# Optimization experiments

Hardware: AMD Instinct MI355X
Metric: run time of the kernel (lower is better)

## Reference

```python
import jax, jax.numpy as jnp
import numpy as np

NSLICES = 4
HID = 512
IN_DIM = 342   # input_shape - 1 (last column is phase)
OUT_DIM = 311
BATCH = 1024


def _cubic(y0, y1, y2, y3, mu):
    mu2 = mu * mu
    mu3 = mu2 * mu
    return ((-0.5 * y0 + 1.5 * y1 - 1.5 * y2 + 0.5 * y3) * mu3
            + (y0 - 2.5 * y1 + 2.0 * y2 - 0.5 * y3) * mu2
            + (-0.5 * y0 + 0.5 * y2) * mu
            + y1)


def setup_inputs() -> dict:
    key = jax.random.key(0)
    kx, k0, k1, k2 = jax.random.split(key, 4)
    x = jax.random.uniform(kx, (BATCH, IN_DIM + 1), dtype=jnp.float32)
    W0 = jax.random.normal(k0, (NSLICES, HID, IN_DIM), dtype=jnp.float32) * 0.1
    W1 = jax.random.normal(k1, (NSLICES, HID, HID), dtype=jnp.float32) * 0.1
    W2 = jax.random.normal(k2, (NSLICES, OUT_DIM, HID), dtype=jnp.float32) * 0.1
    b0 = jnp.zeros((NSLICES, HID), dtype=jnp.float32)
    b1 = jnp.zeros((NSLICES, HID), dtype=jnp.float32)
    b2 = jnp.zeros((NSLICES, OUT_DIM), dtype=jnp.float32)
    return {"x": x, "W0": W0, "W1": W1, "W2": W2, "b0": b0, "b1": b1, "b2": b2}


def reference(x, W0, W1, W2, b0, b1, b2):
    data, phase = x[:, :-1], x[:, -1]          # [B, 342], [B]
    pscale = NSLICES * phase                    # phase in [0,1) -> pscale in [0,4)
    mu = pscale % 1.0                           # [B]
    i1 = pscale.astype(jnp.int32) % NSLICES
    i0 = (i1 - 1) % NSLICES
    i2 = (i1 + 1) % NSLICES
    i3 = (i1 + 2) % NSLICES

    muW = mu[:, None, None]
    mub = mu[:, None]

    # Per-sample interpolated weights/biases (gather 4 slices + cubic blend)
    W0i = _cubic(W0[i0], W0[i1], W0[i2], W0[i3], muW)   # [B, 512, 342]
    W1i = _cubic(W1[i0], W1[i1], W1[i2], W1[i3], muW)   # [B, 512, 512]
    W2i = _cubic(W2[i0], W2[i1], W2[i2], W2[i3], muW)   # [B, 311, 512]
    b0i = _cubic(b0[i0], b0[i1], b0[i2], b0[i3], mub)   # [B, 512]
    b1i = _cubic(b1[i0], b1[i1], b1[i2], b1[i3], mub)   # [B, 512]
    b2i = _cubic(b2[i0], b2[i1], b2[i2], b2[i3], mub)   # [B, 311]

    # 3-layer MLP with per-sample weights (batched GEMV); dropout in eval mode (identity)
    H1 = jax.nn.elu(jnp.einsum('boi,bi->bo', W0i, data) + b0i)
    H2 = jax.nn.elu(jnp.einsum('boi,bi->bo', W1i, H1) + b1i)
    H3 = jnp.einsum('boi,bi->bo', W2i, H2) + b2i
    return H3
```

## Files before the change

kernel.cpp:

```cpp
#include <hip/hip_runtime.h>
#include <hip/hip_fp16.h>
#include <math.h>

typedef _Float16 f16x8 __attribute__((ext_vector_type(8)));
typedef float f32x4 __attribute__((ext_vector_type(4)));

#define NS 4
#define HID 512
#define IN_DIM 342
#define OUT_DIM 311
#define BATCH 1024
#define INP 352
#define K0V (NS*INP)
#define K12V (NS*HID)
#define XROW (IN_DIM+1)

#define OFF_ACOEF 0
#define OFF_X0H   4096
#define OFF_W0H   (OFF_X0H + 720896)
#define OFF_W1H   (OFF_W0H + 360448)
#define OFF_W2H   (OFF_W1H + 524288)
#define OFF_H1X   (OFF_W2H + 327680)
#define OFF_H2X   OFF_X0H

typedef __attribute__((address_space(3))) void lds_t;
typedef __attribute__((address_space(1))) const void gvm_t;
__device__ __forceinline__ void gload16(const void* g, void* l) {
    __builtin_amdgcn_global_load_lds((gvm_t*)g, (lds_t*)l, 16, 0, 0);
}

__global__ __launch_bounds__(256) void prep_all(
    const float* __restrict__ x,
    const float* __restrict__ W0, const float* __restrict__ W1,
    const float* __restrict__ W2,
    float* __restrict__ acoef,
    __half* __restrict__ X0h, __half* __restrict__ W0h,
    __half* __restrict__ W1h, __half* __restrict__ W2h)
{
    const int bid = blockIdx.x;
    const int t = threadIdx.x;
    if (bid < 512) {
        int o = bid;
        for (int k = t; k < K0V; k += 256) {
            int s = k / INP;
            int i = k - s*INP;
            float v = 0.f;
            if (i < IN_DIM) v = W0[((size_t)s*HID + o)*IN_DIM + i];
            W0h[(size_t)o*K0V + k] = __float2half(v);
        }
    } else if (bid < 1024) {
        int o = bid - 512;
        int k = t * 8;
        int s = k >> 9, i = k & 511;
        const float* src = W1 + ((size_t)s*HID + o)*HID + i;
        float4 v0 = *(const float4*)(src);
        float4 v1 = *(const float4*)(src + 4);
        f16x8 h;
        h[0]=(_Float16)v0.x; h[1]=(_Float16)v0.y; h[2]=(_Float16)v0.z; h[3]=(_Float16)v0.w;
        h[4]=(_Float16)v1.x; h[5]=(_Float16)v1.y; h[6]=(_Float16)v1.z; h[7]=(_Float16)v1.w;
        *(f16x8*)(W1h + (size_t)o*K12V + k) = h;
    } else if (bid < 1344) {
        int o = bid - 1024;
        int k = t * 8;
        int s = k >> 9, i = k & 511;
        f16x8 h = {};
        if (o < OUT_DIM) {
            const float* src = W2 + ((size_t)s*OUT_DIM + o)*HID + i;
            float4 v0 = *(const float4*)(src);
            float4 v1 = *(const float4*)(src + 4);
            h[0]=(_Float16)v0.x; h[1]=(_Float16)v0.y; h[2]=(_Float16)v0.z; h[3]=(_Float16)v0.w;
            h[4]=(_Float16)v1.x; h[5]=(_Float16)v1.y; h[6]=(_Float16)v1.z; h[7]=(_Float16)v1.w;
        }
        *(f16x8*)(W2h + (size_t)o*K12V + k) = h;
    } else {
        int b = bid - 1344;
        float phase = x[(size_t)b*XROW + IN_DIM];
        float ps = (float)NS * phase;
        float mu = ps - floorf(ps);
        int i1 = ((int)ps) & (NS-1);
        float mu2 = mu*mu, mu3 = mu2*mu;
        float c1 =  1.5f*mu3 - 2.5f*mu2 + 1.0f;
        float c2 = -1.5f*mu3 + 2.0f*mu2 + 0.5f*mu;
        float c3 =  0.5f*mu3 - 0.5f*mu2;
        float c0 = -0.5f*mu3 +      mu2 - 0.5f*mu;
        if (t < 4) {
            int rel = (t - i1) & 3;
            acoef[b*4 + t] = (rel==0)?c1:(rel==1)?c2:(rel==2)?c3:c0;
        }
        for (int k = t; k < K0V; k += 256) {
            int s = k / INP;
            int i = k - s*INP;
            int rel = (s - i1) & 3;
            float sel = (rel==0)?c1:(rel==1)?c2:(rel==2)?c3:c0;
            float v = (i < IN_DIM) ? x[(size_t)b*XROW + i] * sel : 0.f;
            X0h[(size_t)b*K0V + k] = __float2half(v);
        }
    }
}

template<int LAYER>
__global__ __launch_bounds__(256) void gemm_mfma(
    const __half* __restrict__ A,
    const __half* __restrict__ Bw,
    const float* __restrict__ acoef,
    const float* __restrict__ bias,
    __half* __restrict__ outH,
    float* __restrict__ outF)
{
    constexpr int K  = (LAYER==0) ? K0V : K12V;
    constexpr int NB = (LAYER==2) ? OUT_DIM : HID;
    constexpr int NITER = K / 128;

    __shared__ __align__(16) char lbuf[4][24576];

    const int t    = threadIdx.x;
    const int lane = t & 63;
    const int wid  = t >> 6;
    const int wm   = wid >> 1;
    const int wn   = wid & 1;
    const int m0   = blockIdx.y * 32;
    const int n0   = blockIdx.x * 64;

    const int cS = lane & 15;
    const int r4 = lane >> 4;
    const int rA0 = 4*(wid    ) + r4;
    const int rA1 = 4*(wid + 4) + r4;
    const __half* aSrc0 = A + (size_t)(m0 + rA0)*K + (((cS&8)|((cS&7)^(rA0&7))) * 8);
    const __half* aSrc1 = A + (size_t)(m0 + rA1)*K + (((cS&8)|((cS&7)^(rA1&7))) * 8);
    const int rB0 = 4*(wid     ) + r4;
    const int rB1 = 4*(wid +  4) + r4;
    const int rB2 = 4*(wid +  8) + r4;
    const int rB3 = 4*(wid + 12) + r4;
    const __half* bSrc0 = Bw + (size_t)(n0 + rB0)*K + (((cS&8)|((cS&7)^(rB0&7))) * 8);
    const __half* bSrc1 = Bw + (size_t)(n0 + rB1)*K + (((cS&8)|((cS&7)^(rB1&7))) * 8);
    const __half* bSrc2 = Bw + (size_t)(n0 + rB2)*K + (((cS&8)|((cS&7)^(rB2&7))) * 8);
    const __half* bSrc3 = Bw + (size_t)(n0 + rB3)*K + (((cS&8)|((cS&7)^(rB3&7))) * 8);

    f32x4 acc[2] = {};

    auto stage = [&](int it) {
        char* base = lbuf[it & 3];
        const int ko = it * 128;
        gload16(aSrc0 + ko, base + (wid    )*1024);
        gload16(aSrc1 + ko, base + (wid + 4)*1024);
        gload16(bSrc0 + ko, base + 8192 + (wid     )*1024);
        gload16(bSrc1 + ko, base + 8192 + (wid +  4)*1024);
        gload16(bSrc2 + ko, base + 8192 + (wid +  8)*1024);
        gload16(bSrc3 + ko, base + 8192 + (wid + 12)*1024);
    };

    stage(0);
    stage(1);
    stage(2);

    for (int it = 0; it < NITER; ++it) {
        if (it + 2 < NITER)      asm volatile("s_waitcnt vmcnt(12)" ::: "memory");
        else if (it + 1 < NITER) asm volatile("s_waitcnt vmcnt(6)"  ::: "memory");
        else                     asm volatile("s_waitcnt vmcnt(0)"  ::: "memory");
        __builtin_amdgcn_s_barrier();
        __builtin_amdgcn_sched_barrier(0);
        if (it + 3 < NITER) stage(it + 3);
        const char* sA = lbuf[it & 3];
        const char* sB = sA + 8192;
        #pragma unroll
        for (int kk = 0; kk < 4; ++kk) {
            const int kb = kk*64 + (lane>>4)*16;
            const int rr = wm*16 + (lane&15);
            f16x8 af = *(const f16x8*)(sA + rr*256 + (kb ^ ((rr&7)<<4)));
            #pragma unroll
            for (int ni = 0; ni < 2; ++ni) {
                const int oo = wn*32 + ni*16 + (lane&15);
                f16x8 bf = *(const f16x8*)(sB + oo*256 + (kb ^ ((oo&7)<<4)));
                acc[ni] = __builtin_amdgcn_mfma_f32_16x16x32_f16(af, bf, acc[ni], 0, 0, 0);
            }
        }
    }

    #pragma unroll
    for (int r = 0; r < 4; ++r) {
        const int row = m0 + wm*16 + (lane>>4)*4 + r;
        const float c0 = acoef[row*4+0], c1 = acoef[row*4+1],
                    c2 = acoef[row*4+2], c3 = acoef[row*4+3];
        #pragma unroll
        for (int ni = 0; ni < 2; ++ni) {
            const int col = n0 + wn*32 + ni*16 + (lane&15);
            float v = acc[ni][r];
            if (LAYER == 2) {
                if (col < OUT_DIM) {
                    float bi = c0*bias[col] + c1*bias[NB+col]
                             + c2*bias[2*NB+col] + c3*bias[3*NB+col];
                    outF[(size_t)row*OUT_DIM + col] = v + bi;
                }
            } else {
                float bi = c0*bias[col] + c1*bias[NB+col]
                         + c2*bias[2*NB+col] + c3*bias[3*NB+col];
                v += bi;
                v = (v > 0.f) ? v : expm1f(v);
                size_t o = (size_t)row*K12V + col;
                outH[o        ] = __float2half(c0*v);
                outH[o +   HID] = __float2half(c1*v);
                outH[o + 2*HID] = __float2half(c2*v);
                outH[o + 3*HID] = __float2half(c3*v);
            }
        }
    }
}

extern "C" void kernel_launch(void* const* d_in, const int* in_sizes, int n_in,
                              void* d_out, int out_size, void* d_ws, size_t ws_size,
                              hipStream_t stream) {
    const float* x  = (const float*)d_in[0];
    const float* W0 = (const float*)d_in[1];
    const float* W1 = (const float*)d_in[2];
    const float* W2 = (const float*)d_in[3];
    const float* b0 = (const float*)d_in[4];
    const float* b1 = (const float*)d_in[5];
    const float* b2 = (const float*)d_in[6];
    float* out = (float*)d_out;
    float* ws  = (float*)d_ws;

    float*  acoef = ws + OFF_ACOEF;
    __half* X0h   = (__half*)(ws + OFF_X0H);
    __half* W0h   = (__half*)(ws + OFF_W0H);
    __half* W1h   = (__half*)(ws + OFF_W1H);
    __half* W2h   = (__half*)(ws + OFF_W2H);
    __half* H1x   = (__half*)(ws + OFF_H1X);
    __half* H2x   = (__half*)(ws + OFF_H2X);

    prep_all<<<dim3(2368), dim3(256), 0, stream>>>(x, W0, W1, W2, acoef,
                                                   X0h, W0h, W1h, W2h);

    gemm_mfma<0><<<dim3(HID/64, BATCH/32), dim3(256), 0, stream>>>(
        X0h, W0h, acoef, b0, H1x, nullptr);
    gemm_mfma<1><<<dim3(HID/64, BATCH/32), dim3(256), 0, stream>>>(
        H1x, W1h, acoef, b1, H2x, nullptr);
    gemm_mfma<2><<<dim3(320/64, BATCH/32), dim3(256), 0, stream>>>(
        H2x, W2h, acoef, b2, nullptr, out);
}
```

Before: 38.39 us.

## Overlap W1/W2 fp16 conversion with layer-0 GEMM and vectorize X/W0 prep

The prep kernel now only converts X (scaled by the cubic coefficients) and W0, using 8-wide vectorized loads and stores instead of strided scalar loops. The W1 and W2 fp32-to-fp16 conversion moves into extra blocks appended to the layer-0 GEMM grid, so it runs alongside the GEMM tiles. This shortens the serial prep stage and hides the weight-conversion memory traffic behind layer-0 compute. In exchange, the layer-0 grid becomes heterogeneous, and the conversion blocks still allocate the GEMM's shared-memory footprint.

```diff
diff --git a/kernel.cpp b/kernel.cpp
--- a/kernel.cpp
+++ b/kernel.cpp
@@ -29,71 +29,68 @@
     __builtin_amdgcn_global_load_lds((gvm_t*)g, (lds_t*)l, 16, 0, 0);
 }
 
-__global__ __launch_bounds__(256) void prep_all(
+__global__ __launch_bounds__(256) void prep_xw0(
     const float* __restrict__ x,
-    const float* __restrict__ W0, const float* __restrict__ W1,
-    const float* __restrict__ W2,
+    const float* __restrict__ W0,
     float* __restrict__ acoef,
-    __half* __restrict__ X0h, __half* __restrict__ W0h,
-    __half* __restrict__ W1h, __half* __restrict__ W2h)
+    __half* __restrict__ X0h, __half* __restrict__ W0h)
 {
     const int bid = blockIdx.x;
     const int t = threadIdx.x;
     if (bid < 512) {
         int o = bid;
-        for (int k = t; k < K0V; k += 256) {
-            int s = k / INP;
-            int i = k - s*INP;
-            float v = 0.f;
-            if (i < IN_DIM) v = W0[((size_t)s*HID + o)*IN_DIM + i];
-            W0h[(size_t)o*K0V + k] = __float2half(v);
-        }
-    } else if (bid < 1024) {
-        int o = bid - 512;
-        int k = t * 8;
-        int s = k >> 9, i = k & 511;
-        const float* src = W1 + ((size_t)s*HID + o)*HID + i;
-        float4 v0 = *(const float4*)(src);
-        float4 v1 = *(const float4*)(src + 4);
-        f16x8 h;
-        h[0]=(_Float16)v0.x; h[1]=(_Float16)v0.y; h[2]=(_Float16)v0.z; h[3]=(_Float16)v0.w;
-        h[4]=(_Float16)v1.x; h[5]=(_Float16)v1.y; h[6]=(_Float16)v1.z; h[7]=(_Float16)v1.w;
-        *(f16x8*)(W1h + (size_t)o*K12V + k) = h;
-    } else if (bid < 1344) {
-        int o = bid - 1024;
-        int k = t * 8;
-        int s = k >> 9, i = k & 511;
-        f16x8 h = {};
-        if (o < OUT_DIM) {
-            const float* src = W2 + ((size_t)s*OUT_DIM + o)*HID + i;
-            float4 v0 = *(const float4*)(src);
-            float4 v1 = *(const float4*)(src + 4);
-            h[0]=(_Float16)v0.x; h[1]=(_Float16)v0.y; h[2]=(_Float16)v0.z; h[3]=(_Float16)v0.w;
-            h[4]=(_Float16)v1.x; h[5]=(_Float16)v1.y; h[6]=(_Float16)v1.z; h[7]=(_Float16)v1.w;
-        }
-        *(f16x8*)(W2h + (size_t)o*K12V + k) = h;
+        if (t < 176) {
+            int s = t / 44;
+            int cm = t - s*44;
+            int i = cm * 8;
+            const float* src = W0 + ((size_t)s*HID + o)*IN_DIM + i;
+            f16x8 h;
+            if (i + 8 <= IN_DIM) {
+                float4 v0 = *(const float4*)(src);
+                float4 v1 = *(const float4*)(src + 4);
+                h[0]=(_Float16)v0.x; h[1]=(_Float16)v0.y; h[2]=(_Float16)v0.z; h[3]=(_Float16)v0.w;
+                h[4]=(_Float16)v1.x; h[5]=(_Float16)v1.y; h[6]=(_Float16)v1.z; h[7]=(_Float16)v1.w;
+            } else {
+                #pragma unroll
+                for (int j=0;j<8;++j) h[j] = (_Float16)((i+j < IN_DIM) ? src[j] : 0.f);
+            }
+            *(f16x8*)(W0h + (size_t)o*K0V + t*8) = h;
+        }
     } else {
-        int b = bid - 1344;
+        int b = bid - 512;
         float phase = x[(size_t)b*XROW + IN_DIM];
         float ps = (float)NS * phase;
         float mu = ps - floorf(ps);
         int i1 = ((int)ps) & (NS-1);
         float mu2 = mu*mu, mu3 = mu2*mu;
-        float c1 =  1.5f*mu3 - 2.5f*mu2 + 1.0f;
-        float c2 = -1.5f*mu3 + 2.0f*mu2 + 0.5f*mu;
-        float c3 =  0.5f*mu3 - 0.5f*mu2;
-        float c0 = -0.5f*mu3 +      mu2 - 0.5f*mu;
+        float r0 =  1.5f*mu3 - 2.5f*mu2 + 1.0f;
+        float r1 = -1.5f*mu3 + 2.0f*mu2 + 0.5f*mu;
+        float r2 =  0.5f*mu3 - 0.5f*mu2;
+        float r3 = -0.5f*mu3 +      mu2 - 0.5f*mu;
         if (t < 4) {
             int rel = (t - i1) & 3;
-            acoef[b*4 + t] = (rel==0)?c1:(rel==1)?c2:(rel==2)?c3:c0;
-        }
-        for (int k = t; k < K0V; k += 256) {
-            int s = k / INP;
-            int i = k - s*INP;
+            acoef[b*4 + t] = (rel==0)?r0:(rel==1)?r1:(rel==2)?r2:r3;
+        }
+        if (t < 176) {
+            int s = t / 44;
+            int cm = t - s*44;
+            int i = cm * 8;
             int rel = (s - i1) & 3;
-            float sel = (rel==0)?c1:(rel==1)?c2:(rel==2)?c3:c0;
-            float v = (i < IN_DIM) ? x[(size_t)b*XROW + i] * sel : 0.f;
-            X0h[(size_t)b*K0V + k] = __float2half(v);
+            float sc = (rel==0)?r0:(rel==1)?r1:(rel==2)?r2:r3;
+            const float* src = x + (size_t)b*XROW + i;
+            f16x8 h;
+            if (i + 8 <= IN_DIM) {
+                float4 v0 = *(const float4*)(src);
+                float4 v1 = *(const float4*)(src + 4);
+                h[0]=(_Float16)(v0.x*sc); h[1]=(_Float16)(v0.y*sc);
+                h[2]=(_Float16)(v0.z*sc); h[3]=(_Float16)(v0.w*sc);
+                h[4]=(_Float16)(v1.x*sc); h[5]=(_Float16)(v1.y*sc);
+                h[6]=(_Float16)(v1.z*sc); h[7]=(_Float16)(v1.w*sc);
+            } else {
+                #pragma unroll
+                for (int j=0;j<8;++j) h[j] = (_Float16)((i+j < IN_DIM) ? src[j]*sc : 0.f);
+            }
+            *(f16x8*)(X0h + (size_t)b*K0V + t*8) = h;
         }
     }
 }
@@ -105,21 +102,64 @@
     const float* __restrict__ acoef,
     const float* __restrict__ bias,
     __half* __restrict__ outH,
-    float* __restrict__ outF)
+    float* __restrict__ outF,
+    const float* __restrict__ W1f, const float* __restrict__ W2f,
+    __half* __restrict__ W1h, __half* __restrict__ W2h)
 {
     constexpr int K  = (LAYER==0) ? K0V : K12V;
     constexpr int NB = (LAYER==2) ? OUT_DIM : HID;
     constexpr int NITER = K / 128;
 
+    const int t = threadIdx.x;
+
+    if (LAYER == 0 && blockIdx.x >= 256) {
+        int j = blockIdx.x - 256;
+        int half = t >> 7;
+        int tt = t & 127;
+        int k = tt * 16;
+        int s = k >> 9, i = k & 511;
+        f16x8 h0 = {}, h1 = {};
+        __half* dst;
+        if (j < 256) {
+            int o = j*2 + half;
+            const float* src = W1f + ((size_t)s*HID + o)*HID + i;
+            float4 v0 = *(const float4*)(src);
+            float4 v1 = *(const float4*)(src + 4);
+            float4 v2 = *(const float4*)(src + 8);
+            float4 v3 = *(const float4*)(src + 12);
+            h0[0]=(_Float16)v0.x; h0[1]=(_Float16)v0.y; h0[2]=(_Float16)v0.z; h0[3]=(_Float16)v0.w;
+            h0[4]=(_Float16)v1.x; h0[5]=(_Float16)v1.y; h0[6]=(_Float16)v1.z; h0[7]=(_Float16)v1.w;
+            h1[0]=(_Float16)v2.x; h1[1]=(_Float16)v2.y; h1[2]=(_Float16)v2.z; h1[3]=(_Float16)v2.w;
+            h1[4]=(_Float16)v3.x; h1[5]=(_Float16)v3.y; h1[6]=(_Float16)v3.z; h1[7]=(_Float16)v3.w;
+            dst = W1h + (size_t)o*K12V + k;
+        } else {
+            int o = (j-256)*2 + half;
+            if (o < OUT_DIM) {
+                const float* src = W2f + ((size_t)s*OUT_DIM + o)*HID + i;
+                float4 v0 = *(const float4*)(src);
+                float4 v1 = *(const float4*)(src + 4);
+                float4 v2 = *(const float4*)(src + 8);
+                float4 v3 = *(const float4*)(src + 12);
+                h0[0]=(_Float16)v0.x; h0[1]=(_Float16)v0.y; h0[2]=(_Float16)v0.z; h0[3]=(_Float16)v0.w;
+                h0[4]=(_Float16)v1.x; h0[5]=(_Float16)v1.y; h0[6]=(_Float16)v1.z; h0[7]=(_Float16)v1.w;
+                h1[0]=(_Float16)v2.x; h1[1]=(_Float16)v2.y; h1[2]=(_Float16)v2.z; h1[3]=(_Float16)v2.w;
+                h1[4]=(_Float16)v3.x; h1[5]=(_Float16)v3.y; h1[6]=(_Float16)v3.z; h1[7]=(_Float16)v3.w;
+            }
+            dst = W2h + (size_t)o*K12V + k;
+        }
+        *(f16x8*)(dst)     = h0;
+        *(f16x8*)(dst + 8) = h1;
+        return;
+    }
+
     __shared__ __align__(16) char lbuf[4][24576];
 
-    const int t    = threadIdx.x;
     const int lane = t & 63;
     const int wid  = t >> 6;
     const int wm   = wid >> 1;
     const int wn   = wid & 1;
-    const int m0   = blockIdx.y * 32;
-    const int n0   = blockIdx.x * 64;
+    const int m0   = (LAYER==0) ? (blockIdx.x >> 3)*32 : blockIdx.y * 32;
+    const int n0   = (LAYER==0) ? (blockIdx.x & 7)*64  : blockIdx.x * 64;
 
     const int cS = lane & 15;
     const int r4 = lane >> 4;
@@ -227,13 +267,12 @@
     __half* H1x   = (__half*)(ws + OFF_H1X);
     __half* H2x   = (__half*)(ws + OFF_H2X);
 
-    prep_all<<<dim3(2368), dim3(256), 0, stream>>>(x, W0, W1, W2, acoef,
-                                                   X0h, W0h, W1h, W2h);
-
-    gemm_mfma<0><<<dim3(HID/64, BATCH/32), dim3(256), 0, stream>>>(
-        X0h, W0h, acoef, b0, H1x, nullptr);
+    prep_xw0<<<dim3(1536), dim3(256), 0, stream>>>(x, W0, acoef, X0h, W0h);
+
+    gemm_mfma<0><<<dim3(672), dim3(256), 0, stream>>>(
+        X0h, W0h, acoef, b0, H1x, nullptr, W1, W2, W1h, W2h);
     gemm_mfma<1><<<dim3(HID/64, BATCH/32), dim3(256), 0, stream>>>(
-        H1x, W1h, acoef, b1, H2x, nullptr);
+        H1x, W1h, acoef, b1, H2x, nullptr, nullptr, nullptr, nullptr, nullptr);
     gemm_mfma<2><<<dim3(320/64, BATCH/32), dim3(256), 0, stream>>>(
-        H2x, W2h, acoef, b2, nullptr, out);
-}
+        H2x, W2h, acoef, b2, nullptr, out, nullptr, nullptr, nullptr, nullptr);
+}
```

Result: slower. 39.40 us (+2.6%).

## Load A operand directly into registers and stage only B through LDS

Applied to the files above, without the earlier changes.

The activation (A) tile no longer goes through shared memory. Each wave loads its A fragments straight from global memory into double-buffered registers two iterations ahead, and only the weight (B) tile stays on the 4-deep LDS ring. This cuts LDS footprint and LDS read/write traffic for A, which may allow more resident blocks. The vmcnt waits are recounted for the new mix of loads, and the next B stage is issued after the MFMA work rather than before it. The trade-offs are less coalesced 64-byte row segments for A loads, extra register pressure, and subtler wait accounting.

```diff
diff --git a/kernel.cpp b/kernel.cpp
--- a/kernel.cpp
+++ b/kernel.cpp
@@ -111,7 +111,7 @@
     constexpr int NB = (LAYER==2) ? OUT_DIM : HID;
     constexpr int NITER = K / 128;
 
-    __shared__ __align__(16) char lbuf[4][24576];
+    __shared__ __align__(16) char lbuf[4][16384];
 
     const int t    = threadIdx.x;
     const int lane = t & 63;
@@ -123,10 +123,6 @@
 
     const int cS = lane & 15;
     const int r4 = lane >> 4;
-    const int rA0 = 4*(wid    ) + r4;
-    const int rA1 = 4*(wid + 4) + r4;
-    const __half* aSrc0 = A + (size_t)(m0 + rA0)*K + (((cS&8)|((cS&7)^(rA0&7))) * 8);
-    const __half* aSrc1 = A + (size_t)(m0 + rA1)*K + (((cS&8)|((cS&7)^(rA1&7))) * 8);
     const int rB0 = 4*(wid     ) + r4;
     const int rB1 = 4*(wid +  4) + r4;
     const int rB2 = 4*(wid +  8) + r4;
@@ -136,37 +132,45 @@
     const __half* bSrc2 = Bw + (size_t)(n0 + rB2)*K + (((cS&8)|((cS&7)^(rB2&7))) * 8);
     const __half* bSrc3 = Bw + (size_t)(n0 + rB3)*K + (((cS&8)|((cS&7)^(rB3&7))) * 8);
 
+    const __half* aBase = A + (size_t)(m0 + wm*16 + (lane&15))*K + (lane>>4)*8;
+
     f32x4 acc[2] = {};
-
-    auto stage = [&](int it) {
+    f16x8 aA[4], aB[4];
+
+    auto stageB = [&](int it) {
         char* base = lbuf[it & 3];
         const int ko = it * 128;
-        gload16(aSrc0 + ko, base + (wid    )*1024);
-        gload16(aSrc1 + ko, base + (wid + 4)*1024);
-        gload16(bSrc0 + ko, base + 8192 + (wid     )*1024);
-        gload16(bSrc1 + ko, base + 8192 + (wid +  4)*1024);
-        gload16(bSrc2 + ko, base + 8192 + (wid +  8)*1024);
-        gload16(bSrc3 + ko, base + 8192 + (wid + 12)*1024);
+        gload16(bSrc0 + ko, base + (wid     )*1024);
+        gload16(bSrc1 + ko, base + (wid +  4)*1024);
+        gload16(bSrc2 + ko, base + (wid +  8)*1024);
+        gload16(bSrc3 + ko, base + (wid + 12)*1024);
     };
-
-    stage(0);
-    stage(1);
-    stage(2);
-
-    for (int it = 0; it < NITER; ++it) {
-        if (it + 2 < NITER)      asm volatile("s_waitcnt vmcnt(12)" ::: "memory");
-        else if (it + 1 < NITER) asm volatile("s_waitcnt vmcnt(6)"  ::: "memory");
-        else                     asm volatile("s_waitcnt vmcnt(0)"  ::: "memory");
+    auto loadA = [&](int it, f16x8 (&dst)[4]) {
+        const __half* p = aBase + it*128;
+        #pragma unroll
+        for (int kk = 0; kk < 4; ++kk)
+            dst[kk] = *(const f16x8*)(p + kk*32);
+    };
+
+    loadA(0, aA);
+    if (NITER > 1) loadA(1, aB);
+    stageB(0);
+    stageB(1);
+    stageB(2);
+
+    auto body = [&](int it, f16x8 (&ac)[4]) {
+        if (it == 0)                asm volatile("s_waitcnt vmcnt(8)"  ::: "memory");
+        else if (it == NITER-1)     asm volatile("s_waitcnt vmcnt(4)"  ::: "memory");
+        else if (it == 1)           asm volatile("s_waitcnt vmcnt(12)" ::: "memory");
+        else if (it == NITER-2)     asm volatile("s_waitcnt vmcnt(12)" ::: "memory");
+        else                        asm volatile("s_waitcnt vmcnt(16)" ::: "memory");
         __builtin_amdgcn_s_barrier();
         __builtin_amdgcn_sched_barrier(0);
-        if (it + 3 < NITER) stage(it + 3);
-        const char* sA = lbuf[it & 3];
-        const char* sB = sA + 8192;
+        const char* sB = lbuf[it & 3];
         #pragma unroll
         for (int kk = 0; kk < 4; ++kk) {
             const int kb = kk*64 + (lane>>4)*16;
-            const int rr = wm*16 + (lane&15);
-            f16x8 af = *(const f16x8*)(sA + rr*256 + (kb ^ ((rr&7)<<4)));
+            f16x8 af = ac[kk];
             #pragma unroll
             for (int ni = 0; ni < 2; ++ni) {
                 const int oo = wn*32 + ni*16 + (lane&15);
@@ -174,6 +178,13 @@
                 acc[ni] = __builtin_amdgcn_mfma_f32_16x16x32_f16(af, bf, acc[ni], 0, 0, 0);
             }
         }
+        if (it + 2 < NITER) loadA(it + 2, ac);
+        if (it + 3 < NITER) stageB(it + 3);
+    };
+
+    for (int it = 0; it < NITER; ++it) {
+        if ((it & 1) == 0) body(it, aA);
+        else               body(it, aB);
     }
 
     #pragma unroll
```

New measurement: 69.23 us. +80.3%, slower.
